# Performance work log

Hardware: AMD Instinct MI355X
Metric: run time of the kernel (lower is better)

The kernel has to match this reference:

```python
import jax, jax.numpy as jnp
import numpy as np

B, L, E, K = 64, 1024, 256, 8  # batch, seq_len, d_model, topk (slice width)


def setup_inputs() -> dict:
    key = jax.random.key(0)
    ks = jax.random.split(key, 5)
    s = 1.0 / np.sqrt(E).astype(np.float32)
    return {
        "series": jax.random.normal(ks[0], (B, L, E), jnp.float32),
        "text_series": jax.random.normal(ks[1], (B, L, E), jnp.float32),
        "Wq": jax.random.normal(ks[2], (E, E), jnp.float32) * s,
        "bq": jnp.zeros((E,), jnp.float32),
        "Wk": jax.random.normal(ks[3], (E, E), jnp.float32) * s,
        "bk": jnp.zeros((E,), jnp.float32),
        "Wv": jax.random.normal(ks[4], (E, E), jnp.float32) * s,
        "bv": jnp.zeros((E,), jnp.float32),
    }


def reference(series, text_series, Wq, bq, Wk, bk, Wv, bv):
    Bn, Ln, En = series.shape
    scale = 1.0 / np.sqrt(En).astype(np.float32)
    # nn.Linear: x @ W.T + b
    q = series @ Wq.T + bq            # (B, L, E)
    k = text_series @ Wk.T + bk       # (B, L, E)
    v = text_series @ Wv.T + bv       # (B, L, E)
    # FFT cross-correlation along time axis
    qf = jnp.fft.rfft(q.transpose(0, 2, 1), axis=-1)  # (B, E, L//2+1)
    kf = jnp.fft.rfft(k.transpose(0, 2, 1), axis=-1)
    corr = jnp.fft.irfft(qf * jnp.conj(kf), n=Ln, axis=-1)  # (B, E, L)
    mean_value = corr.mean(axis=1)                           # (B, L)
    # torch.topk(mean over batch, seq_len) == full descending sort of lags
    idx = jnp.argsort(-mean_value.mean(axis=0))              # (L,)
    weights = mean_value[:, idx]                             # (B, L), sorted by lag score
    tmp_corr = jax.nn.softmax(weights * scale, axis=-1)      # (B, L)
    # Original builds cc = concat_i [roll(v, -idx[i], 1) * tmp_corr[:, i]] over all L lags
    # (shape (B, L, L*E)), then returns (cc[..., :K], cc[..., -K:]).
    # With K <= E those slices come solely from the first (i=0) and last (i=L-1) lag blocks.
    out1 = jnp.roll(v, -idx[0], axis=1)[..., :K] * tmp_corr[:, 0][:, None, None]
    out2 = jnp.roll(v, -idx[-1], axis=1)[..., -K:] * tmp_corr[:, -1][:, None, None]
    return (out1, out2)
```

## Files before the change

kernel.cpp:

```cpp
#include <hip/hip_runtime.h>
#include <hip/hip_bf16.h>
#include <math.h>

#define BB 64
#define LL 1024
#define EE 256
#define KK 8
#define EPB 8
#define CHUNKS (EE/EPB)

typedef __attribute__((ext_vector_type(8))) short  bfrag;
typedef __attribute__((ext_vector_type(4))) short  short4v;
typedef __attribute__((ext_vector_type(4))) float  f32x4;

#define MT_KB 10240

#define O_MHI    ((size_t)0)
#define O_MLO    ((size_t)40960)
#define O_BVAUG  ((size_t)81920)
#define O_X      ((size_t)81984)
#define O_KPT    (O_X + (size_t)16777216)
#define O_VSUB   (O_KPT + (size_t)16777216)
#define O_MV     (O_VSUB + (size_t)1048576)
#define O_STATS  (O_MV + (size_t)65536)

__device__ __forceinline__ float2 cmulf(float2 a, float2 b) {
    return make_float2(a.x * b.x - a.y * b.y, a.x * b.y + a.y * b.x);
}

__device__ __forceinline__ int PHY(int i) { return i + (i >> 4); }

__device__ __forceinline__ void splitbf(float x, unsigned short& h, unsigned short& l) {
    __hip_bfloat16 hb = __float2bfloat16(x);
    float hf = __bfloat162float(hb);
    __hip_bfloat16 lb = __float2bfloat16(x - hf);
    h = *(unsigned short*)&hb;
    l = *(unsigned short*)&lb;
}

__device__ __forceinline__ void gload16(const unsigned short* g, unsigned short* l) {
    __builtin_amdgcn_global_load_lds(
        (const __attribute__((address_space(1))) unsigned int*)g,
        (__attribute__((address_space(3))) unsigned int*)l, 16, 0, 0);
}

__device__ __forceinline__ int slot_of(int r, int kq) { return (kq + (r >> 1)) & 3; }

__global__ __launch_bounds__(256) void build_maug(
    const float* __restrict__ Wq, const float* __restrict__ Wk,
    const float* __restrict__ Wv, const float* __restrict__ bv,
    unsigned short* __restrict__ mhiT, unsigned short* __restrict__ mloT,
    float* __restrict__ bvaug) {
    int n = blockIdx.x;
    int j = threadIdx.x;
    float acc;
    if (n < EE) {
        acc = 0.f;
        for (int e = 0; e < EE; ++e)
            acc += Wq[e * EE + n] * Wk[e * EE + j];
    } else {
        int t = n - EE;
        int c = (t < 8) ? t : (240 + t);
        acc = Wv[c * EE + j];
    }
    unsigned short h, l;
    splitbf(acc, h, l);
    const int kb = j >> 5, kq = (j >> 3) & 3;
    const size_t dst = (size_t)kb * MT_KB + n * 32 + slot_of(n, kq) * 8 + (j & 7);
    mhiT[dst] = h;
    mloT[dst] = l;
    if (n == 0 && j < 16) bvaug[j] = bv[(j < 8) ? j : (240 + j)];
}

__global__ __launch_bounds__(256) void split_T(
    const float* __restrict__ T,
    unsigned short* __restrict__ thiT, unsigned short* __restrict__ tloT) {
    const size_t g = (size_t)blockIdx.x * 256 + threadIdx.x;
    const size_t i = g * 8;
    const int s = (int)(i >> 8), k = (int)(i & 255);
    const int kb = k >> 5, kq = (k >> 3) & 3;
    const int st = s >> 6, row = s & 63;
    f32x4 v0 = *(const f32x4*)&T[i];
    f32x4 v1 = *(const f32x4*)&T[i + 4];
    short4v h0, l0, h1, l1;
#pragma unroll
    for (int j = 0; j < 4; ++j) {
        unsigned short h, l;
        splitbf(v0[j], h, l); h0[j] = (short)h; l0[j] = (short)l;
        splitbf(v1[j], h, l); h1[j] = (short)h; l1[j] = (short)l;
    }
    const size_t dst = ((size_t)(st * 8 + kb)) * 2048 + row * 32 + slot_of(row, kq) * 8;
    *(short4v*)&thiT[dst] = h0; *(short4v*)&thiT[dst + 4] = h1;
    *(short4v*)&tloT[dst] = l0; *(short4v*)&tloT[dst + 4] = l1;
}

__global__ __launch_bounds__(256) void transpose_S(
    const float* __restrict__ S, float* __restrict__ St) {
    __shared__ float tile[32][33];
    const int b = blockIdx.z;
    const int l0 = blockIdx.x * 32, e0 = blockIdx.y * 32;
    const int tx = threadIdx.x & 31, ty = threadIdx.x >> 5;
#pragma unroll
    for (int i = 0; i < 32; i += 8)
        tile[ty + i][tx] = S[((size_t)b * LL + l0 + ty + i) * EE + e0 + tx];
    __syncthreads();
#pragma unroll
    for (int i = 0; i < 32; i += 8)
        St[((size_t)b * EE + e0 + ty + i) * LL + l0 + tx] = tile[tx][ty + i];
}

__global__ __launch_bounds__(256, 3) void gemm_mfma(
    const unsigned short* __restrict__ thiT, const unsigned short* __restrict__ tloT,
    const unsigned short* __restrict__ mhiT, const unsigned short* __restrict__ mloT,
    const float* __restrict__ bvaug,
    float* __restrict__ kp_t, float* __restrict__ vsub) {
    __shared__ alignas(16) unsigned short Ah[2048];
    __shared__ alignas(16) unsigned short Al[2048];
    __shared__ alignas(16) unsigned short Bh[10240];
    __shared__ alignas(16) unsigned short Bl[10240];
    const int tid = threadIdx.x;
    const int w = tid >> 6, lane = tid & 63;
    const int lrow = lane & 15, lk = lane >> 4;
    const int st = blockIdx.x;
    const size_t s0 = (size_t)st * 64;
    const int bb = (int)(s0 >> 10), l0 = (int)(s0 & 1023);
    const int gl = w * 64 + lane;

    f32x4 acc[4][4];
    f32x4 acc2[4];
#pragma unroll
    for (int m = 0; m < 4; ++m) {
#pragma unroll
        for (int c = 0; c < 4; ++c) acc[m][c] = (f32x4){0.f, 0.f, 0.f, 0.f};
        acc2[m] = (f32x4){0.f, 0.f, 0.f, 0.f};
    }

    for (int kb = 0; kb < 8; ++kb) {
        __syncthreads();
        const unsigned short* asrcH = thiT + ((size_t)(st * 8 + kb)) * 2048;
        const unsigned short* asrcL = tloT + ((size_t)(st * 8 + kb)) * 2048;
        gload16(asrcH + gl * 8, &Ah[(size_t)w * 512]);
        gload16(asrcL + gl * 8, &Al[(size_t)w * 512]);
        const unsigned short* bsrcH = mhiT + (size_t)kb * MT_KB;
        const unsigned short* bsrcL = mloT + (size_t)kb * MT_KB;
#pragma unroll
        for (int q = 0; q < 5; ++q)
            gload16(bsrcH + q * 2048 + gl * 8, &Bh[q * 2048 + w * 512]);
#pragma unroll
        for (int q = 0; q < 5; ++q)
            gload16(bsrcL + q * 2048 + gl * 8, &Bl[q * 2048 + w * 512]);
        __syncthreads();

        bfrag ah[4], al[4];
#pragma unroll
        for (int m = 0; m < 4; ++m) {
            const int row = m * 16 + lrow;
            const int off = row * 32 + slot_of(row, lk) * 8;
            ah[m] = *(const bfrag*)&Ah[off];
            al[m] = *(const bfrag*)&Al[off];
        }
#pragma unroll
        for (int c = 0; c < 4; ++c) {
            const int n = w * 64 + c * 16 + lrow;
            const int off = n * 32 + slot_of(n, lk) * 8;
            bfrag bh = *(const bfrag*)&Bh[off];
            bfrag bl = *(const bfrag*)&Bl[off];
#pragma unroll
            for (int m = 0; m < 4; ++m) {
                acc[m][c] = __builtin_amdgcn_mfma_f32_16x16x32_bf16(ah[m], bh, acc[m][c], 0, 0, 0);
                acc[m][c] = __builtin_amdgcn_mfma_f32_16x16x32_bf16(ah[m], bl, acc[m][c], 0, 0, 0);
                acc[m][c] = __builtin_amdgcn_mfma_f32_16x16x32_bf16(al[m], bh, acc[m][c], 0, 0, 0);
            }
        }
        if (w == 0) {
            const int n = EE + lrow;
            const int off = n * 32 + slot_of(n, lk) * 8;
            bfrag bh = *(const bfrag*)&Bh[off];
            bfrag bl = *(const bfrag*)&Bl[off];
#pragma unroll
            for (int m = 0; m < 4; ++m) {
                acc2[m] = __builtin_amdgcn_mfma_f32_16x16x32_bf16(ah[m], bh, acc2[m], 0, 0, 0);
                acc2[m] = __builtin_amdgcn_mfma_f32_16x16x32_bf16(ah[m], bl, acc2[m], 0, 0, 0);
                acc2[m] = __builtin_amdgcn_mfma_f32_16x16x32_bf16(al[m], bh, acc2[m], 0, 0, 0);
            }
        }
    }
#pragma unroll
    for (int m = 0; m < 4; ++m) {
        const int srow = m * 16 + lk * 4;
#pragma unroll
        for (int c = 0; c < 4; ++c) {
            const int n = w * 64 + c * 16 + lrow;
            *(f32x4*)&kp_t[((size_t)(bb * EE + n)) * LL + l0 + srow] = acc[m][c];
        }
    }
    if (w == 0) {
        const float bvv = bvaug[lrow];
#pragma unroll
        for (int m = 0; m < 4; ++m) {
            const int srow = m * 16 + lk * 4;
#pragma unroll
            for (int j = 0; j < 4; ++j)
                vsub[(s0 + srow + j) * 16 + lrow] = acc2[m][j] + bvv;
        }
    }
}

template<bool INV>
__device__ __forceinline__ void fft1024_r4(float2* a, float2* b, int tid) {
    float2* src = a;
    float2* dst = b;
#pragma unroll
    for (int t = 0; t < 5; ++t) {
        const int Ns = 1 << (2 * t);
        __syncthreads();
        const int j = tid;
        const int k = j & (Ns - 1);
        float sv, cv;
        __sincosf(-3.14159265358979323846f * (float)k / (float)(2 * Ns), &sv, &cv);
        float2 w1 = make_float2(cv, sv);
        float2 w2 = cmulf(w1, w1);
        float2 w3 = cmulf(w1, w2);
        if (INV) { w1.y = -w1.y; w2.y = -w2.y; w3.y = -w3.y; }
        float2 a0 = src[PHY(j)];
        float2 a1 = cmulf(w1, src[PHY(j + 256)]);
        float2 a2 = cmulf(w2, src[PHY(j + 512)]);
        float2 a3 = cmulf(w3, src[PHY(j + 768)]);
        float2 t0 = make_float2(a0.x + a2.x, a0.y + a2.y);
        float2 t1 = make_float2(a0.x - a2.x, a0.y - a2.y);
        float2 t2 = make_float2(a1.x + a3.x, a1.y + a3.y);
        float2 t3 = make_float2(a1.x - a3.x, a1.y - a3.y);
        float2 u3 = INV ? make_float2(-t3.y, t3.x) : make_float2(t3.y, -t3.x);
        const int base = ((j >> (2 * t)) << (2 * t + 2)) + k;
        dst[PHY(base)]          = make_float2(t0.x + t2.x, t0.y + t2.y);
        dst[PHY(base + Ns)]     = make_float2(t1.x + u3.x, t1.y + u3.y);
        dst[PHY(base + 2 * Ns)] = make_float2(t0.x - t2.x, t0.y - t2.y);
        dst[PHY(base + 3 * Ns)] = make_float2(t1.x - u3.x, t1.y - u3.y);
        float2* tmp = src; src = dst; dst = tmp;
    }
    __syncthreads();
}

__global__ __launch_bounds__(256) void xcorr_kernel(
    float* __restrict__ St, const float* __restrict__ kp_t) {
    __shared__ float2 bufA[1088];
    __shared__ float2 bufB[1088];
    const int tid = threadIdx.x;
    const int b = blockIdx.x / CHUNKS;
    const int chunk = blockIdx.x % CHUNKS;

    float2 p0 = make_float2(0.f, 0.f);
    float2 p1 = make_float2(0.f, 0.f);
    float px2 = 0.f;

    const size_t base = ((size_t)b * EE + (size_t)chunk * EPB) * LL;
    for (int ee = 0; ee < EPB; ++ee) {
        const size_t rbase = base + (size_t)ee * LL;
#pragma unroll
        for (int u = 0; u < 4; ++u) {
            int l = tid + (u << 8);
            bufA[PHY(l)] = make_float2(St[rbase + l], kp_t[rbase + l]);
        }
        fft1024_r4<false>(bufA, bufB, tid);
        {
            float2 A = bufB[PHY(tid)];
            float2 C = bufB[PHY((1024 - tid) & 1023)];
            p0.x += 0.5f * (A.x * C.y + A.y * C.x);
            p0.y += 0.25f * ((A.x * A.x + A.y * A.y) - (C.x * C.x + C.y * C.y));
        }
        {
            int f = tid + 256;
            float2 A = bufB[PHY(f)];
            float2 C = bufB[PHY(1024 - f)];
            p1.x += 0.5f * (A.x * C.y + A.y * C.x);
            p1.y += 0.25f * ((A.x * A.x + A.y * A.y) - (C.x * C.x + C.y * C.y));
        }
        if (tid == 0) {
            float2 A = bufB[PHY(512)];
            px2 += A.x * A.y;
        }
    }
    float2* pp = (float2*)&St[base];
    pp[tid] = p0;
    pp[tid + 256] = p1;
    if (tid == 0) pp[512] = make_float2(px2, 0.f);
}

__global__ __launch_bounds__(256) void ifft_kernel(
    const float* __restrict__ St, float* __restrict__ mv) {
    __shared__ float2 bufA[1088];
    __shared__ float2 bufB[1088];
    const int tid = threadIdx.x;
    const int b = blockIdx.x;
#pragma unroll
    for (int u = 0; u < 2; ++u) {
        int f = tid + (u << 8);
        float2 s = make_float2(0.f, 0.f);
        for (int c = 0; c < CHUNKS; ++c) {
            const float2* pp = (const float2*)&St[((size_t)b * EE + (size_t)c * EPB) * LL];
            float2 v = pp[f];
            s.x += v.x; s.y += v.y;
        }
        if (f == 0) s.y = 0.f;
        bufA[PHY(f)] = s;
        if (f > 0) bufA[PHY(1024 - f)] = make_float2(s.x, -s.y);
    }
    if (tid == 0) {
        float sx = 0.f;
        for (int c = 0; c < CHUNKS; ++c) {
            const float2* pp = (const float2*)&St[((size_t)b * EE + (size_t)c * EPB) * LL];
            sx += pp[512].x;
        }
        bufA[PHY(512)] = make_float2(sx, 0.f);
    }
    fft1024_r4<true>(bufA, bufB, tid);
    const float sc = 1.f / (1024.f * 256.f);
#pragma unroll
    for (int u = 0; u < 4; ++u) {
        int t = tid + (u << 8);
        mv[(size_t)b * LL + t] = bufB[PHY(t)].x * sc;
    }
}

__global__ __launch_bounds__(1024) void argidx_kernel(
    const float* __restrict__ mv, int* __restrict__ istats) {
    __shared__ float smax[1024], smin[1024];
    __shared__ int imax[1024], imin[1024];
    const int t = threadIdx.x;
    float g = 0.f;
    for (int b = 0; b < BB; ++b) g += mv[(size_t)b * LL + t];
    smax[t] = g; smin[t] = g; imax[t] = t; imin[t] = t;
    __syncthreads();
    for (int s = 512; s > 0; s >>= 1) {
        if (t < s) {
            if (smax[t + s] > smax[t] ||
                (smax[t + s] == smax[t] && imax[t + s] < imax[t])) {
                smax[t] = smax[t + s]; imax[t] = imax[t + s];
            }
            if (smin[t + s] < smin[t] ||
                (smin[t + s] == smin[t] && imin[t + s] > imin[t])) {
                smin[t] = smin[t + s]; imin[t] = imin[t + s];
            }
        }
        __syncthreads();
    }
    if (t == 0) { istats[0] = imax[0]; istats[1] = imin[0]; }
}

__global__ __launch_bounds__(256) void softmax_kernel(
    const float* __restrict__ mv, const int* __restrict__ istats,
    float* __restrict__ w01) {
    __shared__ float red[256];
    const int b = blockIdx.x, t = threadIdx.x;
    const float scale = 0.0625f;
    const float* row = mv + (size_t)b * LL;
    float m = -INFINITY;
    for (int i = t; i < LL; i += 256) m = fmaxf(m, row[i]);
    red[t] = m; __syncthreads();
    for (int s = 128; s > 0; s >>= 1) {
        if (t < s) red[t] = fmaxf(red[t], red[t + s]);
        __syncthreads();
    }
    m = red[0]; __syncthreads();
    float sum = 0.f;
    for (int i = t; i < LL; i += 256) sum += expf((row[i] - m) * scale);
    red[t] = sum; __syncthreads();
    for (int s = 128; s > 0; s >>= 1) {
        if (t < s) red[t] += red[t + s];
        __syncthreads();
    }
    if (t == 0) {
        float denom = red[0];
        w01[b]      = expf((row[istats[0]] - m) * scale) / denom;
        w01[BB + b] = expf((row[istats[1]] - m) * scale) / denom;
    }
}

__global__ __launch_bounds__(256) void out_kernel(
    const float* __restrict__ vsub, const int* __restrict__ istats,
    const float* __restrict__ w01, float* __restrict__ out) {
    const int i = blockIdx.x * 256 + threadIdx.x;
    const int half = (i >= BB * LL * KK) ? 1 : 0;
    const int j = i - half * BB * LL * KK;
    const int b = j / (LL * KK);
    const int rem = j % (LL * KK);
    const int l = rem / KK, kk = rem % KK;
    const int sh = istats[half];
    const int lr = (l + sh) & (LL - 1);
    const float w = w01[half * BB + b];
    out[i] = vsub[(size_t)(b * LL + lr) * 16 + half * 8 + kk] * w;
}

extern "C" void kernel_launch(void* const* d_in, const int* in_sizes, int n_in,
                              void* d_out, int out_size, void* d_ws, size_t ws_size,
                              hipStream_t stream) {
    const float* S  = (const float*)d_in[0];
    const float* T  = (const float*)d_in[1];
    const float* Wq = (const float*)d_in[2];
    const float* Wk = (const float*)d_in[4];
    const float* Wv = (const float*)d_in[6];
    const float* bv = (const float*)d_in[7];

    float* ws    = (float*)d_ws;
    unsigned short* mhiT = (unsigned short*)(ws + O_MHI);
    unsigned short* mloT = (unsigned short*)(ws + O_MLO);
    float* bvaug = ws + O_BVAUG;
    unsigned short* thiT = (unsigned short*)(ws + O_X);
    unsigned short* tloT = (unsigned short*)(ws + O_X + 8388608);
    float* st    = ws + O_X;
    float* kp_t  = ws + O_KPT;
    float* vsub  = ws + O_VSUB;
    float* mv    = ws + O_MV;
    float* stats = ws + O_STATS;
    int*   istats = (int*)stats;
    float* w01    = stats + 8;

    build_maug<<<272, 256, 0, stream>>>(Wq, Wk, Wv, bv, mhiT, mloT, bvaug);
    split_T<<<(BB * LL * EE) / (256 * 8), 256, 0, stream>>>(T, thiT, tloT);
    gemm_mfma<<<(BB * LL) / 64, 256, 0, stream>>>(thiT, tloT, mhiT, mloT, bvaug, kp_t, vsub);
    dim3 gT(LL / 32, EE / 32, BB);
    transpose_S<<<gT, 256, 0, stream>>>(S, st);
    xcorr_kernel<<<BB * CHUNKS, 256, 0, stream>>>(st, kp_t);
    ifft_kernel<<<BB, 256, 0, stream>>>(st, mv);
    argidx_kernel<<<1, 1024, 0, stream>>>(mv, istats);
    softmax_kernel<<<BB, 256, 0, stream>>>(mv, istats, w01);
    out_kernel<<<(2 * BB * LL * KK) / 256, 256, 0, stream>>>(vsub, istats, w01, (float*)d_out);
}
```

Before: 166.3 us.

## Run xcorr FFT per single wavefront without barriers, two channels per block

The cross-correlation kernel now uses one 64-lane wavefront per block, and each block handles two embedding channels instead of eight with 256 threads. The FFT is rewritten so each lane does four butterflies per radix-4 stage without __syncthreads, relying on wavefront lockstep, and the last stage's twiddles are derived from one sincos. Loads are vectorized as float4. The aim is to remove barrier stalls and raise the number of blocks in flight. In exchange the ifft kernel must now reduce 128 partial spectra instead of 32, and correctness depends on LDS ordering within a wave with no explicit barrier.

```diff
diff --git a/kernel.cpp b/kernel.cpp
--- a/kernel.cpp
+++ b/kernel.cpp
@@ -6,8 +6,6 @@
 #define LL 1024
 #define EE 256
 #define KK 8
-#define EPB 8
-#define CHUNKS (EE/EPB)
 
 typedef __attribute__((ext_vector_type(8))) short  bfrag;
 typedef __attribute__((ext_vector_type(4))) short  short4v;
@@ -204,6 +202,112 @@
                 vsub[(s0 + srow + j) * 16 + lrow] = acc2[m][j] + bvv;
         }
     }
+}
+
+template<bool INV>
+__device__ __forceinline__ void fft1024_wave(float2* bufA, float2* bufB, int lane) {
+    float2* src = bufA;
+    float2* dst = bufB;
+#pragma unroll
+    for (int t = 0; t < 5; ++t) {
+        const int Ns = 1 << (2 * t);
+        float2 w1b;
+        if (t == 0) {
+            w1b = make_float2(1.f, 0.f);
+        } else {
+            const int k0 = lane & (Ns - 1);
+            float sv, cv;
+            __sincosf(-3.14159265358979323846f * (float)k0 / (float)(2 * Ns), &sv, &cv);
+            w1b = make_float2(cv, INV ? -sv : sv);
+        }
+#pragma unroll
+        for (int u = 0; u < 4; ++u) {
+            const int j = lane + 64 * u;
+            const int k = j & (Ns - 1);
+            float2 a0 = src[PHY(j)];
+            float2 a1s = src[PHY(j + 256)];
+            float2 a2s = src[PHY(j + 512)];
+            float2 a3s = src[PHY(j + 768)];
+            float2 a1, a2, a3;
+            if (t == 0) {
+                a1 = a1s; a2 = a2s; a3 = a3s;
+            } else {
+                float2 w1 = w1b;
+                if (t == 4 && u > 0) {
+                    const float wr = (u == 1) ? 0.923879532511286756f
+                                  : (u == 2) ? 0.707106781186547524f
+                                             : 0.382683432365089772f;
+                    const float wi0 = (u == 1) ? 0.382683432365089772f
+                                   : (u == 2) ? 0.707106781186547524f
+                                              : 0.923879532511286756f;
+                    w1 = cmulf(w1b, make_float2(wr, INV ? wi0 : -wi0));
+                }
+                float2 w2 = cmulf(w1, w1);
+                float2 w3 = cmulf(w1, w2);
+                a1 = cmulf(w1, a1s);
+                a2 = cmulf(w2, a2s);
+                a3 = cmulf(w3, a3s);
+            }
+            float2 t0 = make_float2(a0.x + a2.x, a0.y + a2.y);
+            float2 t1 = make_float2(a0.x - a2.x, a0.y - a2.y);
+            float2 t2 = make_float2(a1.x + a3.x, a1.y + a3.y);
+            float2 t3 = make_float2(a1.x - a3.x, a1.y - a3.y);
+            float2 u3 = INV ? make_float2(-t3.y, t3.x) : make_float2(t3.y, -t3.x);
+            const int base = ((j >> (2 * t)) << (2 * t + 2)) + k;
+            dst[PHY(base)]          = make_float2(t0.x + t2.x, t0.y + t2.y);
+            dst[PHY(base + Ns)]     = make_float2(t1.x + u3.x, t1.y + u3.y);
+            dst[PHY(base + 2 * Ns)] = make_float2(t0.x - t2.x, t0.y - t2.y);
+            dst[PHY(base + 3 * Ns)] = make_float2(t1.x - u3.x, t1.y - u3.y);
+        }
+        float2* tmp = src; src = dst; dst = tmp;
+    }
+}
+
+__global__ __launch_bounds__(64) void xcorr_kernel(
+    float* __restrict__ St, const float* __restrict__ kp_t) {
+    __shared__ float2 bufA[1088];
+    __shared__ float2 bufB[1088];
+    const int lane = threadIdx.x;
+    const int b = blockIdx.x >> 7;
+    const int pair = blockIdx.x & 127;
+    const size_t base = ((size_t)b * EE + 2 * pair) * LL;
+
+    float2 pacc[8];
+#pragma unroll
+    for (int u = 0; u < 8; ++u) pacc[u] = make_float2(0.f, 0.f);
+    float px2 = 0.f;
+
+    for (int ec = 0; ec < 2; ++ec) {
+        const float* sp = St + base + (size_t)ec * LL;
+        const float* kp = kp_t + base + (size_t)ec * LL;
+#pragma unroll
+        for (int u = 0; u < 4; ++u) {
+            const int l0 = 4 * (lane + 64 * u);
+            f32x4 s4 = *(const f32x4*)&sp[l0];
+            f32x4 k4 = *(const f32x4*)&kp[l0];
+#pragma unroll
+            for (int v = 0; v < 4; ++v)
+                bufA[PHY(l0 + v)] = make_float2(s4[v], k4[v]);
+        }
+        fft1024_wave<false>(bufA, bufB, lane);
+#pragma unroll
+        for (int u = 0; u < 8; ++u) {
+            const int f = lane + 64 * u;
+            float2 A = bufB[PHY(f)];
+            float2 C = bufB[PHY((1024 - f) & 1023)];
+            pacc[u].x += 0.5f * (A.x * C.y + A.y * C.x);
+            pacc[u].y += 0.25f * ((A.x * A.x + A.y * A.y) - (C.x * C.x + C.y * C.y));
+        }
+        if (lane == 0) {
+            float2 A = bufB[PHY(512)];
+            px2 += A.x * A.y;
+        }
+    }
+    float2* pp = (float2*)&St[base];
+#pragma unroll
+    for (int u = 0; u < 8; ++u)
+        pp[lane + 64 * u] = pacc[u];
+    if (lane == 0) pp[512] = make_float2(px2, 0.f);
 }
 
 template<bool INV>
@@ -241,51 +345,6 @@
     __syncthreads();
 }
 
-__global__ __launch_bounds__(256) void xcorr_kernel(
-    float* __restrict__ St, const float* __restrict__ kp_t) {
-    __shared__ float2 bufA[1088];
-    __shared__ float2 bufB[1088];
-    const int tid = threadIdx.x;
-    const int b = blockIdx.x / CHUNKS;
-    const int chunk = blockIdx.x % CHUNKS;
-
-    float2 p0 = make_float2(0.f, 0.f);
-    float2 p1 = make_float2(0.f, 0.f);
-    float px2 = 0.f;
-
-    const size_t base = ((size_t)b * EE + (size_t)chunk * EPB) * LL;
-    for (int ee = 0; ee < EPB; ++ee) {
-        const size_t rbase = base + (size_t)ee * LL;
-#pragma unroll
-        for (int u = 0; u < 4; ++u) {
-            int l = tid + (u << 8);
-            bufA[PHY(l)] = make_float2(St[rbase + l], kp_t[rbase + l]);
-        }
-        fft1024_r4<false>(bufA, bufB, tid);
-        {
-            float2 A = bufB[PHY(tid)];
-            float2 C = bufB[PHY((1024 - tid) & 1023)];
-            p0.x += 0.5f * (A.x * C.y + A.y * C.x);
-            p0.y += 0.25f * ((A.x * A.x + A.y * A.y) - (C.x * C.x + C.y * C.y));
-        }
-        {
-            int f = tid + 256;
-            float2 A = bufB[PHY(f)];
-            float2 C = bufB[PHY(1024 - f)];
-            p1.x += 0.5f * (A.x * C.y + A.y * C.x);
-            p1.y += 0.25f * ((A.x * A.x + A.y * A.y) - (C.x * C.x + C.y * C.y));
-        }
-        if (tid == 0) {
-            float2 A = bufB[PHY(512)];
-            px2 += A.x * A.y;
-        }
-    }
-    float2* pp = (float2*)&St[base];
-    pp[tid] = p0;
-    pp[tid + 256] = p1;
-    if (tid == 0) pp[512] = make_float2(px2, 0.f);
-}
-
 __global__ __launch_bounds__(256) void ifft_kernel(
     const float* __restrict__ St, float* __restrict__ mv) {
     __shared__ float2 bufA[1088];
@@ -296,8 +355,8 @@
     for (int u = 0; u < 2; ++u) {
         int f = tid + (u << 8);
         float2 s = make_float2(0.f, 0.f);
-        for (int c = 0; c < CHUNKS; ++c) {
-            const float2* pp = (const float2*)&St[((size_t)b * EE + (size_t)c * EPB) * LL];
+        for (int c = 0; c < 128; ++c) {
+            const float2* pp = (const float2*)&St[((size_t)b * EE + (size_t)c * 2) * LL];
             float2 v = pp[f];
             s.x += v.x; s.y += v.y;
         }
@@ -307,8 +366,8 @@
     }
     if (tid == 0) {
         float sx = 0.f;
-        for (int c = 0; c < CHUNKS; ++c) {
-            const float2* pp = (const float2*)&St[((size_t)b * EE + (size_t)c * EPB) * LL];
+        for (int c = 0; c < 128; ++c) {
+            const float2* pp = (const float2*)&St[((size_t)b * EE + (size_t)c * 2) * LL];
             sx += pp[512].x;
         }
         bufA[PHY(512)] = make_float2(sx, 0.f);
@@ -420,7 +479,7 @@
     gemm_mfma<<<(BB * LL) / 64, 256, 0, stream>>>(thiT, tloT, mhiT, mloT, bvaug, kp_t, vsub);
     dim3 gT(LL / 32, EE / 32, BB);
     transpose_S<<<gT, 256, 0, stream>>>(S, st);
-    xcorr_kernel<<<BB * CHUNKS, 256, 0, stream>>>(st, kp_t);
+    xcorr_kernel<<<BB * 128, 64, 0, stream>>>(st, kp_t);
     ifft_kernel<<<BB, 256, 0, stream>>>(st, mv);
     argidx_kernel<<<1, 1024, 0, stream>>>(mv, istats);
     softmax_kernel<<<BB, 256, 0, stream>>>(mv, istats, w01);
```

Measured after the change: 179.9 us. +8.2%, slower.
